# Performance work log

Hardware: AMD Instinct MI355X
Metric: run time of the kernel (lower is better)

## Reference

```python
import jax, jax.numpy as jnp
import numpy as np

N_NODES = 50000
IN_DIM = 128
OUT_DIM = 2 * IN_DIM  # GCNConv(input_dim, input_dim*2)
N_EDGES = 800000


def setup_inputs() -> dict:
    key = jax.random.key(0)
    k1, k2, k3, k4 = jax.random.split(key, 4)
    x = jax.random.normal(k1, (N_NODES, IN_DIM), dtype=jnp.float32)
    edge_index = jax.random.randint(k2, (N_EDGES, 2), 0, N_NODES, dtype=jnp.int64)
    # GCNConv linear weight [out, in] (applied as x @ W.T) and bias [out]
    scale = 1.0 / np.sqrt(IN_DIM)
    W = jax.random.normal(k3, (OUT_DIM, IN_DIM), dtype=jnp.float32) * scale
    b = jax.random.normal(k4, (OUT_DIM,), dtype=jnp.float32) * 0.01
    return {"x": x, "edge_index": edge_index, "W": W, "b": b}


def reference(x, edge_index, W, b):
    # Faithful to PyG GCNConv: add self-loops, symmetric degree normalization,
    # linear transform, scatter-sum aggregation, bias, then ReLU.
    N = x.shape[0]
    src = edge_index[:, 0]
    dst = edge_index[:, 1]
    loop = jnp.arange(N, dtype=src.dtype)
    src = jnp.concatenate([src, loop])  # [E + N]
    dst = jnp.concatenate([dst, loop])

    h = x @ W.T  # [N, OUT_DIM]

    ones = jnp.ones(dst.shape, dtype=h.dtype)
    deg = jax.ops.segment_sum(ones, dst, num_segments=N)  # in-degree incl. self-loop
    dinv = jnp.where(deg > 0, jax.lax.rsqrt(deg), 0.0)
    norm = dinv[src] * dinv[dst]  # [E + N]

    msg = h[src] * norm[:, None]  # gather + scale, [E+N, OUT_DIM]
    out = jax.ops.segment_sum(msg, dst, num_segments=N) + b  # scatter-add
    return jax.nn.relu(out)
```

## Files before the change

kernel.cpp:

```cpp
#include <hip/hip_runtime.h>

#define N_NODES 50000
#define IN_DIM  128
#define OUT_DIM 256
#define N_EDGES 800000
#define BINA_BLOCKS 128
#define EDGES_PER_BINA 6250
#define XCONV_BLOCKS 782
#define WCONV_BLOCKS 4
#define N_BUCKETS 782
#define BUCKET_CAP 1280

typedef short bf16x8 __attribute__((ext_vector_type(8)));
typedef float f32x4  __attribute__((ext_vector_type(4)));
typedef unsigned short ushort8_t __attribute__((ext_vector_type(8)));

__device__ __forceinline__ unsigned short f2bf(float f) {
    unsigned u = __float_as_uint(f);
    return (unsigned short)((u + 0x7fffu + ((u >> 16) & 1u)) >> 16);
}
__device__ __forceinline__ float bf2f(unsigned short h) {
    return __uint_as_float(((unsigned)h) << 16);
}
__device__ __forceinline__ float blo(unsigned p) { return __uint_as_float(p << 16); }
__device__ __forceinline__ float bhi(unsigned p) { return __uint_as_float(p & 0xffff0000u); }


__global__ __launch_bounds__(1024) void k_prep(const int* __restrict__ ei,
                                               int* __restrict__ bcnt,
                                               unsigned* __restrict__ bucketed,
                                               const float* __restrict__ x,
                                               unsigned short* __restrict__ xb,
                                               const float* __restrict__ W,
                                               unsigned short* __restrict__ Wh,
                                               unsigned short* __restrict__ Wl) {
    __shared__ int hist[N_BUCKETS];
    __shared__ int cursor[N_BUCKETS];
    int b = blockIdx.x, tid = threadIdx.x;
    if (b < BINA_BLOCKS) {
        int base = b * EDGES_PER_BINA;
        for (int t = tid; t < N_BUCKETS; t += 1024) hist[t] = 0;
        __syncthreads();
        for (int e = tid; e < EDGES_PER_BINA; e += 1024) {
            int2 p = *(const int2*)&ei[2 * (base + e)];
            atomicAdd(&hist[p.y >> 6], 1);
        }
        __syncthreads();
        for (int t = tid; t < N_BUCKETS; t += 1024) {
            int cnt = hist[t];
            cursor[t] = t * BUCKET_CAP + (cnt ? atomicAdd(&bcnt[t], cnt) : 0);
        }
        __syncthreads();
        for (int e = tid; e < EDGES_PER_BINA; e += 1024) {
            int2 p = *(const int2*)&ei[2 * (base + e)];
            int bkt = p.y >> 6;
            int pos = atomicAdd(&cursor[bkt], 1);
            if (pos < (bkt + 1) * BUCKET_CAP)
                bucketed[pos] = ((unsigned)(p.y & 63) << 16) | (unsigned)p.x;
        }
    } else if (b < BINA_BLOCKS + XCONV_BLOCKS) {
        int t = (b - BINA_BLOCKS) * 1024 + tid;
        if (t < N_NODES * IN_DIM / 8) {
            int base = t * 8;
            float4 a = *(const float4*)&x[base];
            float4 c = *(const float4*)&x[base + 4];
            ushort8_t o;
            o[0] = f2bf(a.x); o[1] = f2bf(a.y); o[2] = f2bf(a.z); o[3] = f2bf(a.w);
            o[4] = f2bf(c.x); o[5] = f2bf(c.y); o[6] = f2bf(c.z); o[7] = f2bf(c.w);
            *(ushort8_t*)&xb[base] = o;
        }
    } else {
        int t = (b - BINA_BLOCKS - XCONV_BLOCKS) * 1024 + tid;
        int base = t * 8;
        float4 a = *(const float4*)&W[base];
        float4 c = *(const float4*)&W[base + 4];
        ushort8_t h, l;
        h[0] = f2bf(a.x); h[1] = f2bf(a.y); h[2] = f2bf(a.z); h[3] = f2bf(a.w);
        h[4] = f2bf(c.x); h[5] = f2bf(c.y); h[6] = f2bf(c.z); h[7] = f2bf(c.w);
        l[0] = f2bf(a.x - bf2f(h[0])); l[1] = f2bf(a.y - bf2f(h[1]));
        l[2] = f2bf(a.z - bf2f(h[2])); l[3] = f2bf(a.w - bf2f(h[3]));
        l[4] = f2bf(c.x - bf2f(h[4])); l[5] = f2bf(c.y - bf2f(h[5]));
        l[6] = f2bf(c.z - bf2f(h[6])); l[7] = f2bf(c.w - bf2f(h[7]));
        *(ushort8_t*)&Wh[base] = h;
        *(ushort8_t*)&Wl[base] = l;
    }
}


__global__ __launch_bounds__(256) void k_degree(const int* __restrict__ bcnt,
                                                const unsigned* __restrict__ bucketed,
                                                int* __restrict__ counts) {
    __shared__ int h[64];
    int b = blockIdx.x, tid = threadIdx.x;
    if (tid < 64) h[tid] = 0;
    __syncthreads();
    int ecnt = bcnt[b]; if (ecnt > BUCKET_CAP) ecnt = BUCKET_CAP;
    const unsigned* bb = bucketed + b * BUCKET_CAP;
    for (int e = tid; e < ecnt; e += 256)
        atomicAdd(&h[bb[e] >> 16], 1);
    __syncthreads();
    int n = (b << 6) + tid;
    if (tid < 64 && n < N_NODES) counts[n] = h[tid];
}


__global__ __launch_bounds__(512) void k_aggregate(
        const unsigned* __restrict__ xbu, const int* __restrict__ counts,
        const int* __restrict__ bcnt, const unsigned* __restrict__ bucketed,
        unsigned* __restrict__ yh, unsigned* __restrict__ yl) {
    __shared__ int lsrc[BUCKET_CAP];
    __shared__ int ncnt[64], nstart[64], ncur[64];
    int b = blockIdx.x, tid = threadIdx.x;
    int node0 = b << 6;
    if (tid < 64) {
        int n = node0 + tid;
        int c = (n < N_NODES) ? counts[n] : 0;
        ncnt[tid] = c;
        int v = c;
        #pragma unroll
        for (int off = 1; off < 64; off <<= 1) {
            int u = __shfl_up(v, off);
            if (tid >= off) v += u;
        }
        nstart[tid] = v;
        ncur[tid] = v - c;
    }
    __syncthreads();
    int ecnt = bcnt[b]; if (ecnt > BUCKET_CAP) ecnt = BUCKET_CAP;
    const unsigned* bb = bucketed + b * BUCKET_CAP;
    for (int e = tid; e < ecnt; e += 512) {
        unsigned p = bb[e];
        int pos = atomicAdd(&ncur[p >> 16], 1);
        lsrc[pos] = (int)(p & 0xffffu);
    }
    __syncthreads();
    int wv = tid >> 6, lane = tid & 63;
    for (int k = 0; k < 8; ++k) {
        int ln = wv * 8 + k;
        int i = node0 + ln;
        if (i >= N_NODES) break;
        int cnt = ncnt[ln];
        float di = rsqrtf((float)(cnt + 1));
        int end = nstart[ln];
        int start = end - cnt;
        unsigned pself = xbu[i * 64 + lane];
        float sx = di * blo(pself), sy = di * bhi(pself);
        for (int e0 = start; e0 < end; e0 += 64) {
            int ne = end - e0; if (ne > 64) ne = 64;
            int s = 0; float w = 0.f;
            if (lane < ne) {
                s = lsrc[e0 + lane];
                w = rsqrtf((float)(counts[s] + 1));
            }
            int t = 0;
            for (; t + 8 <= ne; t += 8) {
                int s0 = __shfl(s, t),     s1 = __shfl(s, t + 1);
                int s2 = __shfl(s, t + 2), s3 = __shfl(s, t + 3);
                int s4 = __shfl(s, t + 4), s5 = __shfl(s, t + 5);
                int s6 = __shfl(s, t + 6), s7 = __shfl(s, t + 7);
                float w0 = __shfl(w, t),     w1 = __shfl(w, t + 1);
                float w2 = __shfl(w, t + 2), w3 = __shfl(w, t + 3);
                float w4 = __shfl(w, t + 4), w5 = __shfl(w, t + 5);
                float w6 = __shfl(w, t + 6), w7 = __shfl(w, t + 7);
                unsigned p0 = xbu[s0 * 64 + lane], p1 = xbu[s1 * 64 + lane];
                unsigned p2 = xbu[s2 * 64 + lane], p3 = xbu[s3 * 64 + lane];
                unsigned p4 = xbu[s4 * 64 + lane], p5 = xbu[s5 * 64 + lane];
                unsigned p6 = xbu[s6 * 64 + lane], p7 = xbu[s7 * 64 + lane];
                sx += w0 * blo(p0) + w1 * blo(p1) + w2 * blo(p2) + w3 * blo(p3)
                    + w4 * blo(p4) + w5 * blo(p5) + w6 * blo(p6) + w7 * blo(p7);
                sy += w0 * bhi(p0) + w1 * bhi(p1) + w2 * bhi(p2) + w3 * bhi(p3)
                    + w4 * bhi(p4) + w5 * bhi(p5) + w6 * bhi(p6) + w7 * bhi(p7);
            }
            for (; t < ne; ++t) {
                int st = __shfl(s, t); float wt = __shfl(w, t);
                unsigned p = xbu[st * 64 + lane];
                sx += wt * blo(p); sy += wt * bhi(p);
            }
        }
        float vx = di * sx, vy = di * sy;
        unsigned short hx = f2bf(vx), hy = f2bf(vy);
        unsigned short lx = f2bf(vx - bf2f(hx)), ly = f2bf(vy - bf2f(hy));
        yh[i * 64 + lane] = (unsigned)hx | ((unsigned)hy << 16);
        yl[i * 64 + lane] = (unsigned)lx | ((unsigned)ly << 16);
    }
}


#define LDK 136

__global__ __launch_bounds__(256) void k_gemm(
        const unsigned short* __restrict__ yh, const unsigned short* __restrict__ yl,
        const unsigned short* __restrict__ Wh, const unsigned short* __restrict__ Wl,
        const float* __restrict__ bias, float* __restrict__ out) {
    __shared__ unsigned short Ah[64 * LDK], Al[64 * LDK];
    int tid = threadIdx.x;
    int lane = tid & 63;
    int wv = tid >> 6;
    int jb = blockIdx.x * 64;
    int i0 = blockIdx.y * 64;
    int n0 = wv * 16;
    int rl = lane & 15;
    int quad = lane >> 4;

    bf16x8 bh[4], bl[4];
    #pragma unroll
    for (int ks = 0; ks < 4; ++ks) {
        int off = (jb + n0 + rl) * IN_DIM + ks * 32 + quad * 8;
        bh[ks] = *(const bf16x8*)&Wh[off];
        bl[ks] = *(const bf16x8*)&Wl[off];
    }

    #pragma unroll
    for (int it = 0; it < 4; ++it) {
        int g = it * 256 + tid;
        int r = g >> 4;
        int c8 = g & 15;
        int row = i0 + r; if (row >= N_NODES) row = N_NODES - 1;
        int ga = row * IN_DIM + c8 * 8;
        int la = r * LDK + c8 * 8;
        *(bf16x8*)&Ah[la] = *(const bf16x8*)&yh[ga];
        *(bf16x8*)&Al[la] = *(const bf16x8*)&yl[ga];
    }
    __syncthreads();

    f32x4 acc[4] = {{0.f,0.f,0.f,0.f},{0.f,0.f,0.f,0.f},{0.f,0.f,0.f,0.f},{0.f,0.f,0.f,0.f}};
    #pragma unroll
    for (int ks = 0; ks < 4; ++ks) {
        int koff = ks * 32 + quad * 8;
        #pragma unroll
        for (int mt = 0; mt < 4; ++mt) {
            bf16x8 ah = *(bf16x8*)&Ah[(mt * 16 + rl) * LDK + koff];
            bf16x8 al = *(bf16x8*)&Al[(mt * 16 + rl) * LDK + koff];
            acc[mt] = __builtin_amdgcn_mfma_f32_16x16x32_bf16(ah, bh[ks], acc[mt], 0, 0, 0);
            acc[mt] = __builtin_amdgcn_mfma_f32_16x16x32_bf16(ah, bl[ks], acc[mt], 0, 0, 0);
            acc[mt] = __builtin_amdgcn_mfma_f32_16x16x32_bf16(al, bh[ks], acc[mt], 0, 0, 0);
        }
    }

    float bv = bias[jb + n0 + rl];
    #pragma unroll
    for (int mt = 0; mt < 4; ++mt) {
        #pragma unroll
        for (int r = 0; r < 4; ++r) {
            int row = i0 + mt * 16 + quad * 4 + r;
            if (row < N_NODES) {
                float v = acc[mt][r] + bv;
                out[row * OUT_DIM + jb + n0 + rl] = fmaxf(v, 0.f);
            }
        }
    }
}


extern "C" void kernel_launch(void* const* d_in, const int* in_sizes, int n_in,
                              void* d_out, int out_size, void* d_ws, size_t ws_size,
                              hipStream_t stream) {
    const float* x  = (const float*)d_in[0];
    const int*   ei = (const int*)d_in[1];
    const float* W  = (const float*)d_in[2];
    const float* b  = (const float*)d_in[3];
    float* out = (float*)d_out;

    char* ws = (char*)d_ws;
    int*            bcnt     = (int*)(ws + 0);
    int*            counts   = (int*)(ws + 4096);
    unsigned*       bucketed = (unsigned*)(ws + 204800);
    unsigned*       yh       = (unsigned*)(ws + 4208640);
    unsigned*       yl       = (unsigned*)(ws + 17008640);
    unsigned short* xb       = (unsigned short*)(ws + 29808640);
    unsigned short* Wh       = (unsigned short*)(ws + 42608640);
    unsigned short* Wl       = (unsigned short*)(ws + 42674176);

    hipMemsetAsync(bcnt, 0, N_BUCKETS * sizeof(int), stream);

    k_prep<<<BINA_BLOCKS + XCONV_BLOCKS + WCONV_BLOCKS, 1024, 0, stream>>>(
        ei, bcnt, bucketed, x, xb, W, Wh, Wl);
    k_degree<<<N_BUCKETS, 256, 0, stream>>>(bcnt, bucketed, counts);
    k_aggregate<<<N_BUCKETS, 512, 0, stream>>>((const unsigned*)xb, counts, bcnt,
                                               bucketed, yh, yl);
    dim3 g(OUT_DIM / 64, (N_NODES + 63) / 64);
    k_gemm<<<g, 256, 0, stream>>>((const unsigned short*)yh, (const unsigned short*)yl,
                                  Wh, Wl, b, out);
}
```

Measured before the change: 172.5 us.

## Fold source-degree normalization into bf16 x conversion inside degree kernel

The x-to-bf16 conversion moves out of the prep kernel and into the degree kernel, which now prescales each row by its own rsqrt(deg+1) before storing it. The aggregation loop then no longer gathers counts[src] or computes an rsqrt and shuffles a weight per edge; it just sums pre-scaled rows and applies the destination scale at the end. The binning pass also drops to 64 blocks of 12500 edges each. The cost is that x conversion now waits on degree computation, and rounding to bf16 happens after scaling.

```diff
diff --git a/kernel.cpp b/kernel.cpp
--- a/kernel.cpp
+++ b/kernel.cpp
@@ -4,9 +4,8 @@
 #define IN_DIM  128
 #define OUT_DIM 256
 #define N_EDGES 800000
-#define BINA_BLOCKS 128
-#define EDGES_PER_BINA 6250
-#define XCONV_BLOCKS 782
+#define BINA_BLOCKS 64
+#define EDGES_PER_BINA 12500
 #define WCONV_BLOCKS 4
 #define N_BUCKETS 782
 #define BUCKET_CAP 1280
@@ -29,8 +28,6 @@
 __global__ __launch_bounds__(1024) void k_prep(const int* __restrict__ ei,
                                                int* __restrict__ bcnt,
                                                unsigned* __restrict__ bucketed,
-                                               const float* __restrict__ x,
-                                               unsigned short* __restrict__ xb,
                                                const float* __restrict__ W,
                                                unsigned short* __restrict__ Wh,
                                                unsigned short* __restrict__ Wl) {
@@ -58,19 +55,8 @@
             if (pos < (bkt + 1) * BUCKET_CAP)
                 bucketed[pos] = ((unsigned)(p.y & 63) << 16) | (unsigned)p.x;
         }
-    } else if (b < BINA_BLOCKS + XCONV_BLOCKS) {
+    } else {
         int t = (b - BINA_BLOCKS) * 1024 + tid;
-        if (t < N_NODES * IN_DIM / 8) {
-            int base = t * 8;
-            float4 a = *(const float4*)&x[base];
-            float4 c = *(const float4*)&x[base + 4];
-            ushort8_t o;
-            o[0] = f2bf(a.x); o[1] = f2bf(a.y); o[2] = f2bf(a.z); o[3] = f2bf(a.w);
-            o[4] = f2bf(c.x); o[5] = f2bf(c.y); o[6] = f2bf(c.z); o[7] = f2bf(c.w);
-            *(ushort8_t*)&xb[base] = o;
-        }
-    } else {
-        int t = (b - BINA_BLOCKS - XCONV_BLOCKS) * 1024 + tid;
         int base = t * 8;
         float4 a = *(const float4*)&W[base];
         float4 c = *(const float4*)&W[base + 4];
@@ -87,25 +73,51 @@
 }
 
 
-__global__ __launch_bounds__(256) void k_degree(const int* __restrict__ bcnt,
-                                                const unsigned* __restrict__ bucketed,
-                                                int* __restrict__ counts) {
+__global__ __launch_bounds__(512) void k_degxconv(const int* __restrict__ bcnt,
+                                                  const unsigned* __restrict__ bucketed,
+                                                  const float* __restrict__ x,
+                                                  int* __restrict__ counts,
+                                                  unsigned short* __restrict__ xs) {
     __shared__ int h[64];
+    __shared__ float sdinv[64];
     int b = blockIdx.x, tid = threadIdx.x;
+    int node0 = b << 6;
     if (tid < 64) h[tid] = 0;
     __syncthreads();
     int ecnt = bcnt[b]; if (ecnt > BUCKET_CAP) ecnt = BUCKET_CAP;
     const unsigned* bb = bucketed + b * BUCKET_CAP;
-    for (int e = tid; e < ecnt; e += 256)
+    for (int e = tid; e < ecnt; e += 512)
         atomicAdd(&h[bb[e] >> 16], 1);
     __syncthreads();
-    int n = (b << 6) + tid;
-    if (tid < 64 && n < N_NODES) counts[n] = h[tid];
+    if (tid < 64) {
+        int n = node0 + tid;
+        if (n < N_NODES) counts[n] = h[tid];
+        sdinv[tid] = rsqrtf((float)(h[tid] + 1));
+    }
+    __syncthreads();
+    #pragma unroll
+    for (int it = 0; it < 2; ++it) {
+        int g = it * 512 + tid;
+        int nl = g >> 4;
+        int n = node0 + nl;
+        if (n < N_NODES) {
+            float d = sdinv[nl];
+            int base = n * IN_DIM + (g & 15) * 8;
+            float4 a = *(const float4*)&x[base];
+            float4 c = *(const float4*)&x[base + 4];
+            ushort8_t o;
+            o[0] = f2bf(d * a.x); o[1] = f2bf(d * a.y);
+            o[2] = f2bf(d * a.z); o[3] = f2bf(d * a.w);
+            o[4] = f2bf(d * c.x); o[5] = f2bf(d * c.y);
+            o[6] = f2bf(d * c.z); o[7] = f2bf(d * c.w);
+            *(ushort8_t*)&xs[base] = o;
+        }
+    }
 }
 
 
 __global__ __launch_bounds__(512) void k_aggregate(
-        const unsigned* __restrict__ xbu, const int* __restrict__ counts,
+        const unsigned* __restrict__ xsu, const int* __restrict__ counts,
         const int* __restrict__ bcnt, const unsigned* __restrict__ bucketed,
         unsigned* __restrict__ yh, unsigned* __restrict__ yl) {
     __shared__ int lsrc[BUCKET_CAP];
@@ -143,38 +155,30 @@
         float di = rsqrtf((float)(cnt + 1));
         int end = nstart[ln];
         int start = end - cnt;
-        unsigned pself = xbu[i * 64 + lane];
-        float sx = di * blo(pself), sy = di * bhi(pself);
+        unsigned pself = xsu[i * 64 + lane];
+        float sx = blo(pself), sy = bhi(pself);
         for (int e0 = start; e0 < end; e0 += 64) {
             int ne = end - e0; if (ne > 64) ne = 64;
-            int s = 0; float w = 0.f;
-            if (lane < ne) {
-                s = lsrc[e0 + lane];
-                w = rsqrtf((float)(counts[s] + 1));
-            }
+            int s = (lane < ne) ? lsrc[e0 + lane] : 0;
             int t = 0;
             for (; t + 8 <= ne; t += 8) {
                 int s0 = __shfl(s, t),     s1 = __shfl(s, t + 1);
                 int s2 = __shfl(s, t + 2), s3 = __shfl(s, t + 3);
                 int s4 = __shfl(s, t + 4), s5 = __shfl(s, t + 5);
                 int s6 = __shfl(s, t + 6), s7 = __shfl(s, t + 7);
-                float w0 = __shfl(w, t),     w1 = __shfl(w, t + 1);
-                float w2 = __shfl(w, t + 2), w3 = __shfl(w, t + 3);
-                float w4 = __shfl(w, t + 4), w5 = __shfl(w, t + 5);
-                float w6 = __shfl(w, t + 6), w7 = __shfl(w, t + 7);
-                unsigned p0 = xbu[s0 * 64 + lane], p1 = xbu[s1 * 64 + lane];
-                unsigned p2 = xbu[s2 * 64 + lane], p3 = xbu[s3 * 64 + lane];
-                unsigned p4 = xbu[s4 * 64 + lane], p5 = xbu[s5 * 64 + lane];
-                unsigned p6 = xbu[s6 * 64 + lane], p7 = xbu[s7 * 64 + lane];
-                sx += w0 * blo(p0) + w1 * blo(p1) + w2 * blo(p2) + w3 * blo(p3)
-                    + w4 * blo(p4) + w5 * blo(p5) + w6 * blo(p6) + w7 * blo(p7);
-                sy += w0 * bhi(p0) + w1 * bhi(p1) + w2 * bhi(p2) + w3 * bhi(p3)
-                    + w4 * bhi(p4) + w5 * bhi(p5) + w6 * bhi(p6) + w7 * bhi(p7);
+                unsigned p0 = xsu[s0 * 64 + lane], p1 = xsu[s1 * 64 + lane];
+                unsigned p2 = xsu[s2 * 64 + lane], p3 = xsu[s3 * 64 + lane];
+                unsigned p4 = xsu[s4 * 64 + lane], p5 = xsu[s5 * 64 + lane];
+                unsigned p6 = xsu[s6 * 64 + lane], p7 = xsu[s7 * 64 + lane];
+                sx += blo(p0) + blo(p1) + blo(p2) + blo(p3)
+                    + blo(p4) + blo(p5) + blo(p6) + blo(p7);
+                sy += bhi(p0) + bhi(p1) + bhi(p2) + bhi(p3)
+                    + bhi(p4) + bhi(p5) + bhi(p6) + bhi(p7);
             }
             for (; t < ne; ++t) {
-                int st = __shfl(s, t); float wt = __shfl(w, t);
-                unsigned p = xbu[st * 64 + lane];
-                sx += wt * blo(p); sy += wt * bhi(p);
+                int st = __shfl(s, t);
+                unsigned p = xsu[st * 64 + lane];
+                sx += blo(p); sy += bhi(p);
             }
         }
         float vx = di * sx, vy = di * sy;
@@ -267,16 +271,15 @@
     unsigned*       bucketed = (unsigned*)(ws + 204800);
     unsigned*       yh       = (unsigned*)(ws + 4208640);
     unsigned*       yl       = (unsigned*)(ws + 17008640);
-    unsigned short* xb       = (unsigned short*)(ws + 29808640);
+    unsigned short* xs       = (unsigned short*)(ws + 29808640);
     unsigned short* Wh       = (unsigned short*)(ws + 42608640);
     unsigned short* Wl       = (unsigned short*)(ws + 42674176);
 
     hipMemsetAsync(bcnt, 0, N_BUCKETS * sizeof(int), stream);
 
-    k_prep<<<BINA_BLOCKS + XCONV_BLOCKS + WCONV_BLOCKS, 1024, 0, stream>>>(
-        ei, bcnt, bucketed, x, xb, W, Wh, Wl);
-    k_degree<<<N_BUCKETS, 256, 0, stream>>>(bcnt, bucketed, counts);
-    k_aggregate<<<N_BUCKETS, 512, 0, stream>>>((const unsigned*)xb, counts, bcnt,
+    k_prep<<<BINA_BLOCKS + WCONV_BLOCKS, 1024, 0, stream>>>(ei, bcnt, bucketed, W, Wh, Wl);
+    k_degxconv<<<N_BUCKETS, 512, 0, stream>>>(bcnt, bucketed, x, counts, xs);
+    k_aggregate<<<N_BUCKETS, 512, 0, stream>>>((const unsigned*)xs, counts, bcnt,
                                                bucketed, yh, yl);
     dim3 g(OUT_DIM / 64, (N_NODES + 63) / 64);
     k_gemm<<<g, 256, 0, stream>>>((const unsigned short*)yh, (const unsigned short*)yl,
```

Measured after the change: 174.9 us. Within noise of the previous version (+1.4%).
